# Kernel tuning notes

Measured on AMD Instinct MI355X. Metric: run time of the kernel, lower is better.

Reference implementation:

```python
import jax, jax.numpy as jnp
import numpy as np

EPS = 1e-06
GROUPS = ((0, 16), (16, 32), (32, 64))


def setup_inputs() -> dict:
    key = jax.random.key(0)
    k1, k2, k3 = jax.random.split(key, 3)
    B, C, H, W = 32, 64, 128, 128
    x = jax.random.normal(k1, (B, C, H, W), dtype=jnp.float32)
    # stands in for Beta(0.1, 0.1) sample in the torch module
    lmda = jax.random.uniform(k2, (B, 1, 1, 1), dtype=jnp.float32)
    perm = jax.random.permutation(k3, B).astype(jnp.int32)
    return {"x": x, "lmda": lmda, "perm": perm}


def _lower_median(a, axis):
    # torch.median returns the lower of the two middle values for even n
    n = a.shape[axis]
    s = jnp.sort(a, axis=axis)
    return jax.lax.slice_in_dim(s, (n - 1) // 2, (n - 1) // 2 + 1, axis=axis)


def _group_mix(xg, lmda, perm):
    B, Cg, H, W = xg.shape
    mu = jax.lax.stop_gradient(jnp.mean(xg, axis=(2, 3), keepdims=True))
    var = jnp.var(xg, axis=(2, 3), keepdims=True, ddof=1)  # torch unbiased var
    sig = jax.lax.stop_gradient(jnp.sqrt(var + EPS))
    x_normed = (xg - mu) / sig

    med = jax.lax.stop_gradient(_lower_median(_lower_median(xg, 2), 3))  # [B,Cg,1,1]

    flat = xg.reshape(B, Cg, H * W)
    gram = jnp.einsum('bci,bdi->bcd', flat, flat) / (H * W + EPS)
    gram = jax.lax.stop_gradient(gram) + (0.001 + 1e-06) * jnp.eye(Cg, dtype=xg.dtype)

    w, v = jnp.linalg.eigh(gram)
    inv_sqrt = 1.0 / jnp.sqrt(w + EPS)
    whitening = jnp.einsum('bij,bj,bkj->bik', v, inv_sqrt, v)  # [B,Cg,Cg]

    xw = jnp.einsum('bcd,bdn->bcn', whitening, flat - mu.reshape(B, Cg, 1))
    xw = xw.reshape(B, Cg, H, W)

    gram_mix = xw * lmda + xw[perm] * (1.0 - lmda)
    med_mix = med * lmda + med[perm] * (1.0 - lmda)
    return x_normed * gram_mix + med_mix


def reference(x, lmda, perm):
    outs = [_group_mix(x[:, s:e], lmda, perm) for s, e in GROUPS]
    return jnp.concatenate(outs, axis=1)
```

## Files before the change

kernel.cpp:

```cpp
#include <hip/hip_runtime.h>
#include <hip/hip_fp16.h>

#define HWPIX 16384

typedef _Float16 h2 __attribute__((ext_vector_type(2)));
typedef int v2i __attribute__((ext_vector_type(2)));


#define TPAD 130

template<int J>
__device__ inline unsigned shfl_xor_u(unsigned v, int lane) {
  if constexpr (J == 1)
    return (unsigned)__builtin_amdgcn_mov_dpp((int)v, 0xB1, 0xF, 0xF, true);
  else if constexpr (J == 2)
    return (unsigned)__builtin_amdgcn_mov_dpp((int)v, 0x4E, 0xF, 0xF, true);
  else if constexpr (J == 4)
    return (unsigned)__builtin_amdgcn_ds_swizzle((int)v, 0x101F);
  else if constexpr (J == 8)
    return (unsigned)__builtin_amdgcn_ds_swizzle((int)v, 0x201F);
  else if constexpr (J == 16)
    return (unsigned)__builtin_amdgcn_ds_swizzle((int)v, 0x401F);
  else {
#if __has_builtin(__builtin_amdgcn_permlane32_swap)
    v2i r = __builtin_amdgcn_permlane32_swap((int)v, (int)v, false, false);
    return (lane & 32) ? (unsigned)r[0] : (unsigned)r[1];
#else
    return (unsigned)__shfl_xor((int)v, 32);
#endif
  }
}

__device__ inline unsigned pk_min(unsigned a, unsigned b) {
  h2 x = __builtin_bit_cast(h2, a), y = __builtin_bit_cast(h2, b);
  return __builtin_bit_cast(unsigned, __builtin_elementwise_min(x, y));
}
__device__ inline unsigned pk_max(unsigned a, unsigned b) {
  h2 x = __builtin_bit_cast(h2, a), y = __builtin_bit_cast(h2, b);
  return __builtin_bit_cast(unsigned, __builtin_elementwise_max(x, y));
}

template<int CTRL>
__device__ inline unsigned dppmax(unsigned m) {
  unsigned t = (unsigned)__builtin_amdgcn_update_dpp((int)m, (int)m, CTRL, 0xF, 0xF, false);
  return pk_max(m, t);
}

template<int K, int J, int Q>
__device__ inline void bstep(unsigned (&v0)[Q], unsigned (&v1)[Q], const int lane) {
  const bool sel0 = (((lane & J) == 0) == ((lane & K) == 0));
  const int i1 = lane + 64;
  const bool sel1 = (((i1 & J) == 0) == ((i1 & K) == 0));
  unsigned pv[Q];
  #pragma unroll
  for (int q = 0; q < Q; ++q) pv[q] = shfl_xor_u<J>(v0[q], lane);
  #pragma unroll
  for (int q = 0; q < Q; ++q)
    v0[q] = sel0 ? pk_min(v0[q], pv[q]) : pk_max(v0[q], pv[q]);
  #pragma unroll
  for (int q = 0; q < Q; ++q) pv[q] = shfl_xor_u<J>(v1[q], lane);
  #pragma unroll
  for (int q = 0; q < Q; ++q)
    v1[q] = sel1 ? pk_min(v1[q], pv[q]) : pk_max(v1[q], pv[q]);
  if constexpr (J > 1) bstep<K, J / 2, Q>(v0, v1, lane);
}

template<int Q>
__device__ inline void median128h_low(unsigned (&v0)[Q], unsigned (&v1)[Q],
                                      unsigned (&m)[Q], const int lane) {
  bstep<2, 1, Q>(v0, v1, lane);
  bstep<4, 2, Q>(v0, v1, lane);
  bstep<8, 4, Q>(v0, v1, lane);
  bstep<16, 8, Q>(v0, v1, lane);
  bstep<32, 16, Q>(v0, v1, lane);
  bstep<64, 32, Q>(v0, v1, lane);
  #pragma unroll
  for (int q = 0; q < Q; ++q) m[q] = pk_min(v0[q], v1[q]);
  #pragma unroll
  for (int q = 0; q < Q; ++q) m[q] = dppmax<0x111>(m[q]);
  #pragma unroll
  for (int q = 0; q < Q; ++q) m[q] = dppmax<0x112>(m[q]);
  #pragma unroll
  for (int q = 0; q < Q; ++q) m[q] = dppmax<0x114>(m[q]);
  #pragma unroll
  for (int q = 0; q < Q; ++q) m[q] = dppmax<0x118>(m[q]);
  #pragma unroll
  for (int q = 0; q < Q; ++q) m[q] = dppmax<0x142>(m[q]);
  #pragma unroll
  for (int q = 0; q < Q; ++q) m[q] = dppmax<0x143>(m[q]);
}

template<int CTRL>
__device__ inline float fmax_dpp(float m) {
  float t = __builtin_bit_cast(float,
      __builtin_amdgcn_update_dpp(__builtin_bit_cast(int, m),
                                  __builtin_bit_cast(int, m), CTRL, 0xF, 0xF, false));
  return fmaxf(m, t);
}

__device__ inline float median128f_low(float v0, float v1, const int lane) {
  #pragma unroll
  for (int k = 2; k <= 64; k <<= 1) {
    #pragma unroll
    for (int j = k >> 1; j > 0; j >>= 1) {
      const bool sel0 = (((lane & j) == 0) == ((lane & k) == 0));
      const int i1 = lane + 64;
      const bool sel1 = (((i1 & j) == 0) == ((i1 & k) == 0));
      float pv = __shfl_xor(v0, j);
      v0 = sel0 ? fminf(v0, pv) : fmaxf(v0, pv);
      float pw = __shfl_xor(v1, j);
      v1 = sel1 ? fminf(v1, pw) : fmaxf(v1, pw);
    }
  }
  float m = fminf(v0, v1);
  m = fmax_dpp<0x111>(m); m = fmax_dpp<0x112>(m); m = fmax_dpp<0x114>(m);
  m = fmax_dpp<0x118>(m); m = fmax_dpp<0x142>(m); m = fmax_dpp<0x143>(m);
  return m;
}

__global__ __launch_bounds__(512) void stats_kernel(const float* __restrict__ x,
                                                    float* __restrict__ med) {
  __shared__ __half tile[128 * TPAD];
  __shared__ float colmed[128];

  const int bc = blockIdx.x;
  const int tid = threadIdx.x;
  const float* xp = x + (size_t)bc * HWPIX;

  #pragma unroll
  for (int j = 0; j < 8; ++j) {
    int v = tid + j * 512;
    int h = v >> 5;
    int w = (v & 31) * 4;
    float4 val = *reinterpret_cast<const float4*>(xp + (size_t)v * 4);
    __half2* dst = reinterpret_cast<__half2*>(&tile[h * TPAD + w]);
    dst[0] = __floats2half2_rn(val.x, val.y);
    dst[1] = __floats2half2_rn(val.z, val.w);
  }
  __syncthreads();

  const int lane = tid & 63;
  const int wid  = tid >> 6;
  {
    const int w = wid * 16;
    unsigned v0[8], v1[8], m[8];
    #pragma unroll
    for (int q = 0; q < 8; ++q) {
      v0[q] = *reinterpret_cast<const unsigned*>(&tile[lane * TPAD + w + 2 * q]);
      v1[q] = *reinterpret_cast<const unsigned*>(&tile[(lane + 64) * TPAD + w + 2 * q]);
    }
    median128h_low<8>(v0, v1, m, lane);
    if (lane == 63) {
      #pragma unroll
      for (int q = 0; q < 8; ++q) {
        h2 mv = __builtin_bit_cast(h2, m[q]);
        colmed[w + 2 * q]     = (float)mv.x;
        colmed[w + 2 * q + 1] = (float)mv.y;
      }
    }
  }
  __syncthreads();
  if (wid == 0) {
    float m = median128f_low(colmed[lane], colmed[lane + 64], lane);
    if (lane == 63) med[bc] = m;
  }
}

template<int CG>
__global__ __launch_bounds__(256) void gram_kernel(const float* __restrict__ x,
                                                   float* __restrict__ gpart,
                                                   float* __restrict__ rspart) {
  constexpr int QT   = CG / 4;
  constexpr int TPG  = QT * QT;
  constexpr int PQ   = 256 / TPG;
  constexpr int SUBP = 256 / PQ;
  constexpr int THR  = 256 / CG;
  __shared__ float tile[CG][260];

  const int b = blockIdx.z;
  const int g = blockIdx.y;
  const int s    = (CG == 16) ? g * 16  : 32;
  const int goff = (CG == 16) ? g * 256 : 512;
  const int chunk = blockIdx.x;
  const int k0 = chunk * 1024;
  const int tid = threadIdx.x;
  const int pq = tid / TPG;
  const int t  = tid % TPG;
  const int ty = t / QT, tx = t % QT;
  const int r0 = ty * 4, c0 = tx * 4;
  const int rrow = tid / THR;
  const int rseg = tid % THR;

  const float* xb = x + (((size_t)(b * 64 + s)) << 14) + k0;
  float acc[4][4] = {};
  float rsum = 0.f;

  for (int sc = 0; sc < 4; ++sc) {
    #pragma unroll
    for (int v = tid; v < CG * 64; v += 256) {
      int r = v >> 6;
      int p4 = (v & 63) * 4;
      *reinterpret_cast<float4*>(&tile[r][p4]) =
          *reinterpret_cast<const float4*>(xb + ((size_t)r << 14) + sc * 256 + p4);
    }
    __syncthreads();
    const int pb0 = pq * SUBP;
    #pragma unroll
    for (int p = pb0; p < pb0 + SUBP; p += 4) {
      float4 a[4], bb[4];
      #pragma unroll
      for (int i = 0; i < 4; ++i) a[i]  = *reinterpret_cast<const float4*>(&tile[r0 + i][p]);
      #pragma unroll
      for (int i = 0; i < 4; ++i) bb[i] = *reinterpret_cast<const float4*>(&tile[c0 + i][p]);
      #pragma unroll
      for (int i = 0; i < 4; ++i)
        #pragma unroll
        for (int j = 0; j < 4; ++j)
          acc[i][j] += a[i].x * bb[j].x + a[i].y * bb[j].y +
                       a[i].z * bb[j].z + a[i].w * bb[j].w;
    }
    #pragma unroll
    for (int i = 0; i < CG / 4; ++i) {
      const float4 v = *reinterpret_cast<const float4*>(&tile[rrow][rseg * CG + i * 4]);
      rsum += v.x + v.y + v.z + v.w;
    }
    __syncthreads();
  }

  #pragma unroll
  for (int j = 1; j < THR; j <<= 1) rsum += __shfl_xor(rsum, j);
  if (rseg == 0) rspart[chunk * 2048 + b * 64 + s + rrow] = rsum;

  float* scratch = reinterpret_cast<float*>(tile);
  #pragma unroll
  for (int i = 0; i < 4; ++i)
    #pragma unroll
    for (int j = 0; j < 4; ++j)
      scratch[(t * PQ + pq) * 16 + i * 4 + j] = acc[i][j];
  __syncthreads();
  if (pq == 0) {
    float* gp = gpart + (size_t)(chunk * 32 + b) * 1536 + goff;
    #pragma unroll
    for (int i = 0; i < 4; ++i)
      #pragma unroll
      for (int j = 0; j < 4; ++j) {
        float v = 0.f;
        for (int q = 0; q < PQ; ++q) v += scratch[(t * PQ + q) * 16 + i * 4 + j];
        gp[(r0 + i) * CG + (c0 + j)] = v;
      }
  }
}

template<int CG>
__device__ __forceinline__ void ns_impl(const float* __restrict__ gpart,
                                        const float* __restrict__ rspart,
                                        float* __restrict__ mu,
                                        float* __restrict__ rsig,
                                        float* __restrict__ wht,
                                        const int b, const int g, char* smem) {
  constexpr int NE = CG * CG;
  constexpr int PADC = CG + 4;
  constexpr int MS = CG * PADC;
  float* Y0 = (float*)smem;
  float* Z0 = Y0 + MS;
  float* Y1 = Z0 + MS;
  float* Z1 = Y1 + MS;
  float* T  = Z1 + MS;
  float* red = T + MS;

  const int s    = (CG == 16) ? g * 16  : 32;
  const int goff = (CG == 16) ? g * 256 : 512;
  const int tid = threadIdx.x;
  const float invHW = (float)(1.0 / (16384.0 + 1e-6));

  for (int e = tid; e < NE; e += 256) {
    int r = e / CG, c = e % CG;
    float v = 0.f;
    #pragma unroll
    for (int ch = 0; ch < 16; ++ch)
      v += gpart[(size_t)(ch * 32 + b) * 1536 + goff + e];
    T[r * PADC + c] = v;
  }
  __syncthreads();

  if (tid < CG) {
    float rs = 0.f;
    #pragma unroll
    for (int ch = 0; ch < 16; ++ch) rs += rspart[ch * 2048 + b * 64 + s + tid];
    const float diag = T[tid * PADC + tid];
    const float mean = rs * (1.0f / HWPIX);
    const float var = (diag - rs * mean) / (float)(HWPIX - 1);
    mu[b * 64 + s + tid] = mean;
    rsig[b * 64 + s + tid] = rsqrtf(var + 1e-6f);
  }
  __syncthreads();

  float ssq = 0.f;
  for (int e = tid; e < NE; e += 256) {
    int r = e / CG, c = e % CG;
    float v = T[r * PADC + c] * invHW + ((r == c) ? 0.001002f : 0.0f);
    T[r * PADC + c] = v;
    ssq += v * v;
  }
  red[tid] = ssq;
  __syncthreads();
  for (int off = 128; off > 0; off >>= 1) {
    if (tid < off) red[tid] += red[tid + off];
    __syncthreads();
  }
  const float cn = sqrtf(red[0]);
  const float icn = 1.0f / cn;
  for (int e = tid; e < NE; e += 256) {
    int r = e / CG, c = e % CG;
    Y0[r * PADC + c] = T[r * PADC + c] * icn;
    Z0[r * PADC + c] = (r == c) ? 1.0f : 0.0f;
  }
  __syncthreads();

  constexpr int ACT = NE / 4;
  const int r  = tid / (CG / 4);
  const int c0 = (tid % (CG / 4)) * 4;

  for (int it = 0; it < 12; ++it) {
    float* Yi = (it & 1) ? Y1 : Y0;
    float* Zi = (it & 1) ? Z1 : Z0;
    float* Yo = (it & 1) ? Y0 : Y1;
    float* Zo = (it & 1) ? Z0 : Z1;
    if (tid < ACT) {
      float ax = 0.f, ay = 0.f, az = 0.f, aw = 0.f;
      #pragma unroll
      for (int k = 0; k < CG; ++k) {
        float zr = Zi[r * PADC + k];
        const float4 yk = *reinterpret_cast<const float4*>(&Yi[k * PADC + c0]);
        ax += zr * yk.x; ay += zr * yk.y; az += zr * yk.z; aw += zr * yk.w;
      }
      float4 tv;
      tv.x = ((r == c0 + 0) ? 3.f : 0.f) - ax;
      tv.y = ((r == c0 + 1) ? 3.f : 0.f) - ay;
      tv.z = ((r == c0 + 2) ? 3.f : 0.f) - az;
      tv.w = ((r == c0 + 3) ? 3.f : 0.f) - aw;
      *reinterpret_cast<float4*>(&T[r * PADC + c0]) = tv;
    }
    __syncthreads();
    if (tid < ACT) {
      float yx = 0.f, yy = 0.f, yz = 0.f, yw = 0.f;
      float zx = 0.f, zy = 0.f, zz = 0.f, zw = 0.f;
      #pragma unroll
      for (int k = 0; k < CG; ++k) {
        float yr = Yi[r * PADC + k];
        float tr = T[r * PADC + k];
        const float4 tk = *reinterpret_cast<const float4*>(&T[k * PADC + c0]);
        const float4 zk = *reinterpret_cast<const float4*>(&Zi[k * PADC + c0]);
        yx += yr * tk.x; yy += yr * tk.y; yz += yr * tk.z; yw += yr * tk.w;
        zx += tr * zk.x; zy += tr * zk.y; zz += tr * zk.z; zw += tr * zk.w;
      }
      *reinterpret_cast<float4*>(&Yo[r * PADC + c0]) =
          make_float4(0.5f * yx, 0.5f * yy, 0.5f * yz, 0.5f * yw);
      *reinterpret_cast<float4*>(&Zo[r * PADC + c0]) =
          make_float4(0.5f * zx, 0.5f * zy, 0.5f * zz, 0.5f * zw);
    }
    __syncthreads();
  }

  const float wscale = rsqrtf(cn);
  for (int e = tid; e < NE; e += 256) {
    int r2 = e / CG, c2 = e % CG;
    wht[b * 1536 + goff + e] = Z0[r2 * PADC + c2] * wscale;
  }
}

__global__ __launch_bounds__(256) void ns_all(const float* __restrict__ gpart,
                                              const float* __restrict__ rspart,
                                              float* __restrict__ mu,
                                              float* __restrict__ rsig,
                                              float* __restrict__ wht) {
  __shared__ __align__(16) char smem[5 * 32 * 36 * 4 + 1024];
  const int bid = blockIdx.x;
  if (bid < 64) ns_impl<16>(gpart, rspart, mu, rsig, wht, bid >> 1, bid & 1, smem);
  else          ns_impl<32>(gpart, rspart, mu, rsig, wht, bid - 64, 0, smem);
}

template<int CG>
__device__ __forceinline__ void apply_impl2(
    const float* __restrict__ x, const float* __restrict__ lmda,
    const int* __restrict__ perm, const float* __restrict__ mu,
    const float* __restrict__ rsig, const float* __restrict__ med,
    const float* __restrict__ wht, float* __restrict__ out,
    float* W1, float* W2, float* mu1, float* mu2, float* rs1, float* mm) {
  const int b = blockIdx.z;
  const int g = blockIdx.y;
  const int s    = (CG == 16) ? g * 16  : 32;
  const int goff = (CG == 16) ? g * 256 : 512;
  const int tid = threadIdx.x;
  const int pb = perm[b];
  const float lam = lmda[b];
  const float oml = 1.0f - lam;

  for (int e = tid; e < CG * CG; e += 256) {
    W1[e] = wht[b  * 1536 + goff + e] * lam;
    W2[e] = wht[pb * 1536 + goff + e] * oml;
  }
  if (tid < CG) {
    int ch1 = b * 64 + s + tid, ch2 = pb * 64 + s + tid;
    mu1[tid] = mu[ch1];
    mu2[tid] = mu[ch2];
    rs1[tid] = rsig[ch1];
    mm[tid]  = lam * med[ch1] + oml * med[ch2];
  }
  __syncthreads();

  const int p = blockIdx.x * 512 + tid * 2;
  const float* xb1 = x + (((size_t)(b  * 64 + s)) << 14) + p;
  const float* xb2 = x + (((size_t)(pb * 64 + s)) << 14) + p;
  float* ob = out + (((size_t)(b * 64 + s)) << 14) + p;

  float2 xv1[CG], xv2[CG];
  #pragma unroll
  for (int d = 0; d < CG; ++d) xv1[d] = *reinterpret_cast<const float2*>(xb1 + ((size_t)d << 14));
  #pragma unroll
  for (int d = 0; d < CG; ++d) xv2[d] = *reinterpret_cast<const float2*>(xb2 + ((size_t)d << 14));
  #pragma unroll
  for (int d = 0; d < CG; ++d) {
    xv1[d].x -= mu1[d]; xv1[d].y -= mu1[d];
    xv2[d].x -= mu2[d]; xv2[d].y -= mu2[d];
  }

  float2 acc[CG] = {};
  #pragma unroll
  for (int d = 0; d < CG; ++d) {
    #pragma unroll
    for (int c = 0; c < CG; ++c) {
      const float w1 = W1[d * CG + c];
      const float w2 = W2[d * CG + c];
      acc[c].x += w1 * xv1[d].x;
      acc[c].y += w1 * xv1[d].y;
      acc[c].x += w2 * xv2[d].x;
      acc[c].y += w2 * xv2[d].y;
    }
  }
  #pragma unroll
  for (int c = 0; c < CG; ++c) {
    float2 v;
    v.x = xv1[c].x * rs1[c] * acc[c].x + mm[c];
    v.y = xv1[c].y * rs1[c] * acc[c].y + mm[c];
    unsigned long long uv = __builtin_bit_cast(unsigned long long, v);
    __builtin_nontemporal_store(uv,
        reinterpret_cast<unsigned long long*>(ob + ((size_t)c << 14)));
  }
}

__global__ __launch_bounds__(256, 4) void apply16(
    const float* __restrict__ x, const float* __restrict__ lmda,
    const int* __restrict__ perm, const float* __restrict__ mu,
    const float* __restrict__ rsig, const float* __restrict__ med,
    const float* __restrict__ wht, float* __restrict__ out) {
  __shared__ float W1[256], W2[256];
  __shared__ float mu1[16], mu2[16], rs1[16], mm[16];
  apply_impl2<16>(x, lmda, perm, mu, rsig, med, wht, out, W1, W2, mu1, mu2, rs1, mm);
}

__global__ __launch_bounds__(256, 2) void apply32(
    const float* __restrict__ x, const float* __restrict__ lmda,
    const int* __restrict__ perm, const float* __restrict__ mu,
    const float* __restrict__ rsig, const float* __restrict__ med,
    const float* __restrict__ wht, float* __restrict__ out) {
  __shared__ float W1[1024], W2[1024];
  __shared__ float mu1[32], mu2[32], rs1[32], mm[32];
  apply_impl2<32>(x, lmda, perm, mu, rsig, med, wht, out, W1, W2, mu1, mu2, rs1, mm);
}

extern "C" void kernel_launch(void* const* d_in, const int* in_sizes, int n_in,
                              void* d_out, int out_size, void* d_ws, size_t ws_size,
                              hipStream_t stream) {
  const float* x    = (const float*)d_in[0];
  const float* lmda = (const float*)d_in[1];
  const int*   perm = (const int*)d_in[2];
  float* out = (float*)d_out;
  float* ws  = (float*)d_ws;

  float* mu     = ws;
  float* rsig   = ws + 2048;
  float* med    = ws + 4096;
  float* wht    = ws + 6144;
  float* rspart = ws + 55296;
  float* gpart  = ws + 88064;

  gram_kernel<16><<<dim3(16, 2, 32), 256, 0, stream>>>(x, gpart, rspart);
  gram_kernel<32><<<dim3(16, 1, 32), 256, 0, stream>>>(x, gpart, rspart);

  stats_kernel<<<2048, 512, 0, stream>>>(x, med);

  ns_all<<<96, 256, 0, stream>>>(gpart, rspart, mu, rsig, wht);

  apply16<<<dim3(32, 2, 32), 256, 0, stream>>>(x, lmda, perm, mu, rsig, med, wht, out);
  apply32<<<dim3(32, 1, 32), 256, 0, stream>>>(x, lmda, perm, mu, rsig, med, wht, out);
}
```

Baseline: 235.4 us.

## Split apply32 output channels across blocks and widen apply16 to 4-pixel vectors

The apply stage is restructured. apply16 now processes 4 pixels per thread with float4 loads and stores and launches half as many blocks. apply32 is split into two blocks per batch along the output-channel axis, each holding a 32x16 slice of the whitening weights and 16 accumulators, which cuts register pressure. The catch is that each apply32 block still reads all 32 input channels for both the sample and its permuted partner, so reads of x for that group double.

```diff
diff --git a/kernel.cpp b/kernel.cpp
--- a/kernel.cpp
+++ b/kernel.cpp
@@ -5,6 +5,8 @@
 
 typedef _Float16 h2 __attribute__((ext_vector_type(2)));
 typedef int v2i __attribute__((ext_vector_type(2)));
+typedef float f2 __attribute__((ext_vector_type(2)));
+typedef float f4 __attribute__((ext_vector_type(4)));
 
 
 #define TPAD 130
@@ -380,83 +382,62 @@
   else          ns_impl<32>(gpart, rspart, mu, rsig, wht, bid - 64, 0, smem);
 }
 
-template<int CG>
-__device__ __forceinline__ void apply_impl2(
-    const float* __restrict__ x, const float* __restrict__ lmda,
-    const int* __restrict__ perm, const float* __restrict__ mu,
-    const float* __restrict__ rsig, const float* __restrict__ med,
-    const float* __restrict__ wht, float* __restrict__ out,
-    float* W1, float* W2, float* mu1, float* mu2, float* rs1, float* mm) {
-  const int b = blockIdx.z;
-  const int g = blockIdx.y;
-  const int s    = (CG == 16) ? g * 16  : 32;
-  const int goff = (CG == 16) ? g * 256 : 512;
-  const int tid = threadIdx.x;
-  const int pb = perm[b];
-  const float lam = lmda[b];
-  const float oml = 1.0f - lam;
-
-  for (int e = tid; e < CG * CG; e += 256) {
-    W1[e] = wht[b  * 1536 + goff + e] * lam;
-    W2[e] = wht[pb * 1536 + goff + e] * oml;
-  }
-  if (tid < CG) {
-    int ch1 = b * 64 + s + tid, ch2 = pb * 64 + s + tid;
-    mu1[tid] = mu[ch1];
-    mu2[tid] = mu[ch2];
-    rs1[tid] = rsig[ch1];
-    mm[tid]  = lam * med[ch1] + oml * med[ch2];
-  }
-  __syncthreads();
-
-  const int p = blockIdx.x * 512 + tid * 2;
-  const float* xb1 = x + (((size_t)(b  * 64 + s)) << 14) + p;
-  const float* xb2 = x + (((size_t)(pb * 64 + s)) << 14) + p;
-  float* ob = out + (((size_t)(b * 64 + s)) << 14) + p;
-
-  float2 xv1[CG], xv2[CG];
-  #pragma unroll
-  for (int d = 0; d < CG; ++d) xv1[d] = *reinterpret_cast<const float2*>(xb1 + ((size_t)d << 14));
-  #pragma unroll
-  for (int d = 0; d < CG; ++d) xv2[d] = *reinterpret_cast<const float2*>(xb2 + ((size_t)d << 14));
-  #pragma unroll
-  for (int d = 0; d < CG; ++d) {
-    xv1[d].x -= mu1[d]; xv1[d].y -= mu1[d];
-    xv2[d].x -= mu2[d]; xv2[d].y -= mu2[d];
-  }
-
-  float2 acc[CG] = {};
-  #pragma unroll
-  for (int d = 0; d < CG; ++d) {
-    #pragma unroll
-    for (int c = 0; c < CG; ++c) {
-      const float w1 = W1[d * CG + c];
-      const float w2 = W2[d * CG + c];
-      acc[c].x += w1 * xv1[d].x;
-      acc[c].y += w1 * xv1[d].y;
-      acc[c].x += w2 * xv2[d].x;
-      acc[c].y += w2 * xv2[d].y;
-    }
-  }
-  #pragma unroll
-  for (int c = 0; c < CG; ++c) {
-    float2 v;
-    v.x = xv1[c].x * rs1[c] * acc[c].x + mm[c];
-    v.y = xv1[c].y * rs1[c] * acc[c].y + mm[c];
-    unsigned long long uv = __builtin_bit_cast(unsigned long long, v);
-    __builtin_nontemporal_store(uv,
-        reinterpret_cast<unsigned long long*>(ob + ((size_t)c << 14)));
-  }
-}
-
-__global__ __launch_bounds__(256, 4) void apply16(
+__global__ __launch_bounds__(256, 2) void apply16(
     const float* __restrict__ x, const float* __restrict__ lmda,
     const int* __restrict__ perm, const float* __restrict__ mu,
     const float* __restrict__ rsig, const float* __restrict__ med,
     const float* __restrict__ wht, float* __restrict__ out) {
   __shared__ float W1[256], W2[256];
   __shared__ float mu1[16], mu2[16], rs1[16], mm[16];
-  apply_impl2<16>(x, lmda, perm, mu, rsig, med, wht, out, W1, W2, mu1, mu2, rs1, mm);
+
+  const int b = blockIdx.z;
+  const int g = blockIdx.y;
+  const int s = g * 16, goff = g * 256;
+  const int tid = threadIdx.x;
+  const int pb = perm[b];
+  const float lam = lmda[b];
+  const float oml = 1.0f - lam;
+
+  if (tid < 256) {
+    W1[tid] = wht[b  * 1536 + goff + tid] * lam;
+    W2[tid] = wht[pb * 1536 + goff + tid] * oml;
+  }
+  if (tid < 16) {
+    int ch1 = b * 64 + s + tid, ch2 = pb * 64 + s + tid;
+    mu1[tid] = mu[ch1];
+    mu2[tid] = mu[ch2];
+    rs1[tid] = rsig[ch1];
+    mm[tid]  = lam * med[ch1] + oml * med[ch2];
+  }
+  __syncthreads();
+
+  const int p = blockIdx.x * 1024 + tid * 4;
+  const float* xb1 = x + (((size_t)(b  * 64 + s)) << 14) + p;
+  const float* xb2 = x + (((size_t)(pb * 64 + s)) << 14) + p;
+  float* ob = out + (((size_t)(b * 64 + s)) << 14) + p;
+
+  f4 xv1[16], xv2[16];
+  #pragma unroll
+  for (int d = 0; d < 16; ++d) xv1[d] = *reinterpret_cast<const f4*>(xb1 + ((size_t)d << 14));
+  #pragma unroll
+  for (int d = 0; d < 16; ++d) xv2[d] = *reinterpret_cast<const f4*>(xb2 + ((size_t)d << 14));
+  #pragma unroll
+  for (int d = 0; d < 16; ++d) { xv1[d] -= mu1[d]; xv2[d] -= mu2[d]; }
+
+  f4 acc[16] = {};
+  #pragma unroll
+  for (int d = 0; d < 16; ++d) {
+    #pragma unroll
+    for (int c = 0; c < 16; ++c) {
+      acc[c] += W1[d * 16 + c] * xv1[d];
+      acc[c] += W2[d * 16 + c] * xv2[d];
+    }
+  }
+  #pragma unroll
+  for (int c = 0; c < 16; ++c) {
+    f4 v = xv1[c] * rs1[c] * acc[c] + mm[c];
+    __builtin_nontemporal_store(v, reinterpret_cast<f4*>(ob + ((size_t)c << 14)));
+  }
 }
 
 __global__ __launch_bounds__(256, 2) void apply32(
@@ -464,9 +445,60 @@
     const int* __restrict__ perm, const float* __restrict__ mu,
     const float* __restrict__ rsig, const float* __restrict__ med,
     const float* __restrict__ wht, float* __restrict__ out) {
-  __shared__ float W1[1024], W2[1024];
-  __shared__ float mu1[32], mu2[32], rs1[32], mm[32];
-  apply_impl2<32>(x, lmda, perm, mu, rsig, med, wht, out, W1, W2, mu1, mu2, rs1, mm);
+  __shared__ float W1h[512], W2h[512];
+  __shared__ float mu1[32], mu2[32], rs1[16], mm[16];
+
+  const int b = blockIdx.z;
+  const int h = blockIdx.y;
+  const int tid = threadIdx.x;
+  const int pb = perm[b];
+  const float lam = lmda[b];
+  const float oml = 1.0f - lam;
+
+  for (int e = tid; e < 512; e += 256) {
+    int d = e >> 4, ch = e & 15;
+    W1h[e] = wht[b  * 1536 + 512 + d * 32 + h * 16 + ch] * lam;
+    W2h[e] = wht[pb * 1536 + 512 + d * 32 + h * 16 + ch] * oml;
+  }
+  if (tid < 32) {
+    mu1[tid] = mu[b  * 64 + 32 + tid];
+    mu2[tid] = mu[pb * 64 + 32 + tid];
+  }
+  if (tid < 16) {
+    int cg = 32 + h * 16 + tid;
+    rs1[tid] = rsig[b * 64 + cg];
+    mm[tid]  = lam * med[b * 64 + cg] + oml * med[pb * 64 + cg];
+  }
+  __syncthreads();
+
+  const int p = blockIdx.x * 512 + tid * 2;
+  const float* xb1 = x + (((size_t)(b  * 64 + 32)) << 14) + p;
+  const float* xb2 = x + (((size_t)(pb * 64 + 32)) << 14) + p;
+  float* ob = out + (((size_t)(b * 64 + 32)) << 14) + p;
+
+  f2 xv1[32], xv2[32];
+  #pragma unroll
+  for (int d = 0; d < 32; ++d) xv1[d] = *reinterpret_cast<const f2*>(xb1 + ((size_t)d << 14));
+  #pragma unroll
+  for (int d = 0; d < 32; ++d) xv2[d] = *reinterpret_cast<const f2*>(xb2 + ((size_t)d << 14));
+  #pragma unroll
+  for (int d = 0; d < 32; ++d) { xv1[d] -= mu1[d]; xv2[d] -= mu2[d]; }
+
+  f2 acc[16] = {};
+  #pragma unroll
+  for (int d = 0; d < 32; ++d) {
+    #pragma unroll
+    for (int c = 0; c < 16; ++c) {
+      acc[c] += W1h[d * 16 + c] * xv1[d];
+      acc[c] += W2h[d * 16 + c] * xv2[d];
+    }
+  }
+  #pragma unroll
+  for (int c = 0; c < 16; ++c) {
+    const int cg = h * 16 + c;
+    f2 v = xv1[cg] * rs1[c] * acc[c] + mm[c];
+    __builtin_nontemporal_store(v, reinterpret_cast<f2*>(ob + ((size_t)cg << 14)));
+  }
 }
 
 extern "C" void kernel_launch(void* const* d_in, const int* in_sizes, int n_in,
@@ -492,6 +524,6 @@
 
   ns_all<<<96, 256, 0, stream>>>(gpart, rspart, mu, rsig, wht);
 
-  apply16<<<dim3(32, 2, 32), 256, 0, stream>>>(x, lmda, perm, mu, rsig, med, wht, out);
-  apply32<<<dim3(32, 1, 32), 256, 0, stream>>>(x, lmda, perm, mu, rsig, med, wht, out);
-}
+  apply16<<<dim3(16, 2, 32), 256, 0, stream>>>(x, lmda, perm, mu, rsig, med, wht, out);
+  apply32<<<dim3(32, 2, 32), 256, 0, stream>>>(x, lmda, perm, mu, rsig, med, wht, out);
+}
```

Measured after the change: 258.0 us. +9.6%, slower.
